# Optimization experiments

Measured on AMD Instinct MI355X. Metric: run time of the kernel, lower is better.

## Reference

```python
import jax, jax.numpy as jnp
import numpy as np

NUM_NODES = 50000
NUM_EDGES = 800000
INPUT_DIM = 256
OUTPUT_DIM = 256
NUM_HEADS = 8
HEAD_DIM = OUTPUT_DIM // NUM_HEADS


def setup_inputs() -> dict:
    key = jax.random.key(0)
    ks = jax.random.split(key, 14)
    x = jax.random.normal(ks[0], (NUM_NODES, INPUT_DIM), dtype=jnp.float32)
    edge_index = jax.random.randint(ks[1], (2, NUM_EDGES), 0, NUM_NODES, dtype=jnp.int32)
    # timestamps in seconds over ~11.5 days so log1p(|dt|/3600) is informative
    edge_time = jax.random.uniform(ks[2], (NUM_EDGES,), dtype=jnp.float32) * 1e6
    node_time = jax.random.uniform(ks[3], (NUM_NODES,), dtype=jnp.float32) * 1e6
    s_in = 1.0 / np.sqrt(INPUT_DIM)
    s_out = 1.0 / np.sqrt(OUTPUT_DIM)
    s_t = 1.0 / np.sqrt(2.0)
    Wq = jax.random.uniform(ks[4], (INPUT_DIM, OUTPUT_DIM), jnp.float32, -s_in, s_in)
    bq = jax.random.uniform(ks[5], (OUTPUT_DIM,), jnp.float32, -s_in, s_in)
    Wk = jax.random.uniform(ks[6], (INPUT_DIM, OUTPUT_DIM), jnp.float32, -s_in, s_in)
    bk = jax.random.uniform(ks[7], (OUTPUT_DIM,), jnp.float32, -s_in, s_in)
    Wv = jax.random.uniform(ks[8], (INPUT_DIM, OUTPUT_DIM), jnp.float32, -s_in, s_in)
    bv = jax.random.uniform(ks[9], (OUTPUT_DIM,), jnp.float32, -s_in, s_in)
    Wt = jax.random.uniform(ks[10], (2, NUM_HEADS), jnp.float32, -s_t, s_t)
    bt = jax.random.uniform(ks[11], (NUM_HEADS,), jnp.float32, -s_t, s_t)
    Wo = jax.random.uniform(ks[12], (OUTPUT_DIM, OUTPUT_DIM), jnp.float32, -s_out, s_out)
    bo = jax.random.uniform(ks[13], (OUTPUT_DIM,), jnp.float32, -s_out, s_out)
    return {"x": x, "edge_index": edge_index, "edge_time": edge_time, "node_time": node_time,
            "Wq": Wq, "bq": bq, "Wk": Wk, "bk": bk, "Wv": Wv, "bv": bv,
            "Wt": Wt, "bt": bt, "Wo": Wo, "bo": bo}


def reference(x, edge_index, edge_time, node_time, Wq, bq, Wk, bk, Wv, bv, Wt, bt, Wo, bo):
    n = x.shape[0]
    q = (x @ Wq + bq).reshape(n, NUM_HEADS, HEAD_DIM)
    k = (x @ Wk + bk).reshape(n, NUM_HEADS, HEAD_DIM)
    v = (x @ Wv + bv).reshape(n, NUM_HEADS, HEAD_DIM)
    src, dst = edge_index[0], edge_index[1]
    # temporal features per edge
    time_diff = edge_time - node_time[dst]
    time_features = jnp.stack(
        [jnp.sign(time_diff), jnp.log1p(jnp.abs(time_diff) / 3600.0)], axis=-1)  # [E, 2]
    temporal_weights = time_features @ Wt + bt  # [E, H]
    scale = HEAD_DIM ** -0.5
    scores = jnp.einsum('ehd,ehd->eh', q[dst], k[src]) * scale + temporal_weights  # [E, H]
    # softmax over ALL edges per head (dim=0), as in the original
    alpha = jax.nn.softmax(scores, axis=0)  # [E, H]
    msg = alpha[..., None] * v[src]  # [E, H, D]
    out = jax.ops.segment_sum(msg, dst, num_segments=n)  # [N, H, D]
    out = out.reshape(n, OUTPUT_DIM)
    return out @ Wo + bo
```

## Files before the change

### kernel.cpp

```cpp
#include <hip/hip_runtime.h>
#include <hip/hip_bf16.h>

#define NUM_NODES 50000
#define NUM_EDGES 800000
#define NUM_HEADS 8
#define HEAD_DIM 32
#define SCAN_BLOCKS 49
#define NCHUNK32 1563

typedef unsigned short ushort8 __attribute__((ext_vector_type(8)));
typedef float f32x4 __attribute__((ext_vector_type(4)));
typedef __bf16 bf16x8 __attribute__((ext_vector_type(8)));
typedef _Float16 h2 __attribute__((ext_vector_type(2)));

union BF8 { ushort8 u; bf16x8 b; };
union H8 { ushort8 u; h2 h[4]; };

#if defined(__has_builtin)
#if __has_builtin(__builtin_amdgcn_fdot2)
#define FDOT2(a, b, c) __builtin_amdgcn_fdot2((a), (b), (c), false)
#endif
#endif
#ifndef FDOT2
#define FDOT2(a, b, c) ((float)(a)[0] * (float)(b)[0] + (float)(a)[1] * (float)(b)[1] + (c))
#endif

__device__ __forceinline__ unsigned float_to_key(float f) {
    int i = __float_as_int(f);
    return (i >= 0) ? ((unsigned)i | 0x80000000u) : ~(unsigned)i;
}
__device__ __forceinline__ float key_to_float(unsigned u) {
    unsigned b = (u & 0x80000000u) ? (u & 0x7fffffffu) : ~u;
    return __int_as_float((int)b);
}
__device__ __forceinline__ float bf2f(unsigned short u) {
    return __uint_as_float(((unsigned)u) << 16);
}
__device__ __forceinline__ unsigned short f2bf(float f) {
    unsigned u = __float_as_uint(f);
    unsigned r = (u + 0x7fffu + ((u >> 16) & 1u)) >> 16;
    return (unsigned short)r;
}
__device__ __forceinline__ unsigned short f2h(float f) {
    _Float16 h = (_Float16)f;
    return *(unsigned short*)&h;
}

__global__ __launch_bounds__(256) void deg_kernel(const int* __restrict__ dst_idx, int* __restrict__ deg) {
    int e = blockIdx.x * 256 + threadIdx.x;
    if (e < NUM_EDGES) atomicAdd(&deg[dst_idx[e]], 1);
}

__global__ __launch_bounds__(1024) void scanA_kernel(
    const int* __restrict__ deg, int* __restrict__ offs, int* __restrict__ blocksum)
{
    __shared__ int buf[1024];
    int tid = threadIdx.x;
    int i = blockIdx.x * 1024 + tid;
    int v = (i < NUM_NODES) ? deg[i] : 0;
    buf[tid] = v;
    __syncthreads();
    for (int off = 1; off < 1024; off <<= 1) {
        int t = (tid >= off) ? buf[tid - off] : 0;
        __syncthreads();
        buf[tid] += t;
        __syncthreads();
    }
    if (i < NUM_NODES) offs[i] = buf[tid] - v;
    if (tid == 1023) blocksum[blockIdx.x] = buf[1023];
}

__global__ __launch_bounds__(64) void scanB_kernel(
    const int* __restrict__ blocksum, int* __restrict__ carry, int* __restrict__ offs)
{
    if (threadIdx.x == 0) {
        int acc = 0;
        for (int b = 0; b < SCAN_BLOCKS; b++) { carry[b] = acc; acc += blocksum[b]; }
        offs[NUM_NODES] = acc;
    }
}

__global__ __launch_bounds__(256) void scanC_kernel(
    int* __restrict__ offs, const int* __restrict__ carry, int* __restrict__ cursor)
{
    int i = blockIdx.x * 256 + threadIdx.x;
    if (i < NUM_NODES) {
        int v = offs[i] + carry[i >> 10];
        offs[i] = v;
        cursor[i] = v;
    }
}

__global__ __launch_bounds__(256) void fill3_kernel(
    const int* __restrict__ src_idx, const int* __restrict__ dst_idx,
    const float* __restrict__ edge_time, const float* __restrict__ node_time,
    int* __restrict__ cursor, int2* __restrict__ sd, float2* __restrict__ tf,
    int* __restrict__ src_s)
{
    int e = blockIdx.x * 256 + threadIdx.x;
    if (e < NUM_EDGES) {
        int d = dst_idx[e];
        int s = src_idx[e];
        int pos = atomicAdd(&cursor[d], 1);
        int2 v; v.x = s; v.y = d;
        sd[pos] = v;
        src_s[pos] = s;
        float td = edge_time[e] - node_time[d];
        float t0 = (td > 0.f) ? 1.f : ((td < 0.f) ? -1.f : 0.f);
        float t1 = log1pf(fabsf(td) * (1.f / 3600.f));
        tf[pos] = make_float2(t0, t1);
    }
}

__global__ __launch_bounds__(256) void wtrans_kernel(
    const float* __restrict__ Wq, const float* __restrict__ Wk,
    const float* __restrict__ Wv, const float* __restrict__ Wo,
    unsigned short* __restrict__ Wt)
{
    __shared__ float t[64][65];
    int nb = blockIdx.x * 64;
    int kb = blockIdx.y * 64;
    int g = nb >> 8;
    const float* W = (g == 0) ? Wq : (g == 1) ? Wk : (g == 2) ? Wv : Wo;
    int n0 = nb & 255;
    int tx = threadIdx.x & 63;
    int ty = threadIdx.x >> 6;
#pragma unroll
    for (int i = 0; i < 16; i++) {
        int k = i * 4 + ty;
        t[tx][k] = W[(size_t)(kb + k) * 256 + n0 + tx];
    }
    __syncthreads();
#pragma unroll
    for (int i = 0; i < 16; i++) {
        int n = i * 4 + ty;
        Wt[(size_t)(nb + n) * 256 + kb + tx] = f2bf(t[n][tx]);
    }
}

__global__ __launch_bounds__(256) void wpack_kernel(
    const unsigned short* __restrict__ Wt, unsigned short* __restrict__ Wpk)
{
    int gid = blockIdx.x * 256 + threadIdx.x;
    int lane = gid & 63;
    int fragidx = gid >> 6;
    int c2 = fragidx & 7;
    int nf = (fragidx >> 3) & 3;
    int cb = (fragidx >> 5) & 3;
    int g = fragidx >> 7;
    int l16 = lane & 15;
    int kg = lane >> 4;
    int n_col = g * 256 + cb * 64 + nf * 16 + l16;
    int k0 = c2 * 32 + kg * 8;
    ushort8 v = *(const ushort8*)(Wt + (size_t)n_col * 256 + k0);
    *(ushort8*)(Wpk + (size_t)gid * 8) = v;
}

__global__ __launch_bounds__(256) void gemm_qkv_mfma7(
    const float* __restrict__ A, int M,
    const unsigned short* __restrict__ Wpk,
    const float* __restrict__ b0, const float* __restrict__ b1, const float* __restrict__ b2,
    unsigned short* __restrict__ O0, unsigned short* __restrict__ O1, unsigned short* __restrict__ O2)
{
    __shared__ unsigned short As[64 * 256];
    int tid = threadIdx.x;
    int rowbase = blockIdx.x * 64;

    {
        int rsub = tid >> 6;
        int c4 = (tid & 63) * 4;
        int cchunk = (tid & 63) >> 1;
        int sub = (tid & 1);
#pragma unroll
        for (int it = 0; it < 16; it++) {
            int row = it * 4 + rsub;
            int grow = rowbase + row;
            float4 av = make_float4(0.f, 0.f, 0.f, 0.f);
            if (grow < M) av = *(const float4*)(A + (size_t)grow * 256 + c4);
            ushort4 o;
            o.x = f2bf(av.x); o.y = f2bf(av.y); o.z = f2bf(av.z); o.w = f2bf(av.w);
            unsigned byte = row * 512 + ((unsigned)(cchunk ^ (row & 7)) << 4) + sub * 8;
            *(ushort4*)((char*)As + byte) = o;
        }
    }
    __syncthreads();

    int lane = tid & 63;
    int wid = tid >> 6;
    int l16 = lane & 15;
    int kg = lane >> 4;

#pragma unroll
    for (int p = 0; p < 3; p++) {
        const float* bias = (p == 0) ? b0 : (p == 1) ? b1 : b2;
        unsigned short* O = (p == 0) ? O0 : (p == 1) ? O1 : O2;

        f32x4 acc[4][4];
#pragma unroll
        for (int m = 0; m < 4; m++)
#pragma unroll
            for (int n = 0; n < 4; n++) acc[m][n] = (f32x4)(0.0f);

        const ushort8* wbase = (const ushort8*)(Wpk + ((size_t)(p * 4 + wid) * 2048 + lane) * 8);

#pragma unroll
        for (int c2 = 0; c2 < 8; c2++) {
            bf16x8 wfr[4];
#pragma unroll
            for (int n = 0; n < 4; n++) {
                BF8 t; t.u = wbase[(n * 8 + c2) * 64];
                wfr[n] = t.b;
            }
            bf16x8 afr[4];
#pragma unroll
            for (int m = 0; m < 4; m++) {
                int row = m * 16 + l16;
                int cchunk = (c2 * 4 + kg) ^ (row & 7);
                BF8 t;
                t.u = *(const ushort8*)((const char*)As + row * 512 + (cchunk << 4));
                afr[m] = t.b;
            }
#pragma unroll
            for (int m = 0; m < 4; m++)
#pragma unroll
                for (int n = 0; n < 4; n++)
                    acc[m][n] = __builtin_amdgcn_mfma_f32_16x16x32_bf16(wfr[n], afr[m], acc[m][n], 0, 0, 0);
        }

#pragma unroll
        for (int m = 0; m < 4; m++) {
            int node = rowbase + m * 16 + l16;
            if (node >= M) continue;
#pragma unroll
            for (int n = 0; n < 4; n++) {
                int lc = wid * 64 + n * 16 + kg * 4;
                float4 bv = *(const float4*)(bias + lc);
                ushort4 o;
                if (p < 2) {
                    o.x = f2h(acc[m][n][0] + bv.x);
                    o.y = f2h(acc[m][n][1] + bv.y);
                    o.z = f2h(acc[m][n][2] + bv.z);
                    o.w = f2h(acc[m][n][3] + bv.w);
                } else {
                    o.x = f2bf(acc[m][n][0] + bv.x);
                    o.y = f2bf(acc[m][n][1] + bv.y);
                    o.z = f2bf(acc[m][n][2] + bv.z);
                    o.w = f2bf(acc[m][n][3] + bv.w);
                }
                int hh = lc >> 5, dd = lc & 31;
                *(ushort4*)(O + ((size_t)hh * NUM_NODES + node) * 32 + dd) = o;
            }
        }
    }
}

__global__ __launch_bounds__(256) void gemm_out_mfma6(
    const unsigned short* __restrict__ aggb, int M,
    const unsigned short* __restrict__ Wpk,
    const float* __restrict__ bias, const float* __restrict__ kscale,
    float* __restrict__ C)
{
    __shared__ unsigned short As[64 * 256];
    int tid = threadIdx.x;
    int rowbase = blockIdx.x * 64;

    {
        int rsub = tid >> 6;
        int c4 = (tid & 63) * 4;
        int cchunk = (tid & 63) >> 1;
        int sub = (tid & 1);
        int hh = c4 >> 5, dd = c4 & 31;
        float ks = kscale[hh];
#pragma unroll
        for (int it = 0; it < 16; it++) {
            int row = it * 4 + rsub;
            int grow = rowbase + row;
            ushort4 av = make_ushort4(0, 0, 0, 0);
            if (grow < M) av = *(const ushort4*)(aggb + ((size_t)hh * NUM_NODES + grow) * 32 + dd);
            ushort4 o;
            o.x = f2bf(bf2f(av.x) * ks); o.y = f2bf(bf2f(av.y) * ks);
            o.z = f2bf(bf2f(av.z) * ks); o.w = f2bf(bf2f(av.w) * ks);
            unsigned byte = row * 512 + ((unsigned)(cchunk ^ (row & 7)) << 4) + sub * 8;
            *(ushort4*)((char*)As + byte) = o;
        }
    }
    __syncthreads();

    int lane = tid & 63;
    int wid = tid >> 6;
    int l16 = lane & 15;
    int kg = lane >> 4;

    f32x4 acc[4][4];
#pragma unroll
    for (int m = 0; m < 4; m++)
#pragma unroll
        for (int n = 0; n < 4; n++) acc[m][n] = (f32x4)(0.0f);

    const ushort8* wbase = (const ushort8*)(Wpk + ((size_t)wid * 2048 + lane) * 8);

#pragma unroll
    for (int c2 = 0; c2 < 8; c2++) {
        bf16x8 wfr[4];
#pragma unroll
        for (int n = 0; n < 4; n++) {
            BF8 t; t.u = wbase[(n * 8 + c2) * 64];
            wfr[n] = t.b;
        }
        bf16x8 afr[4];
#pragma unroll
        for (int m = 0; m < 4; m++) {
            int row = m * 16 + l16;
            int cchunk = (c2 * 4 + kg) ^ (row & 7);
            BF8 t;
            t.u = *(const ushort8*)((const char*)As + row * 512 + (cchunk << 4));
            afr[m] = t.b;
        }
#pragma unroll
        for (int m = 0; m < 4; m++)
#pragma unroll
            for (int n = 0; n < 4; n++)
                acc[m][n] = __builtin_amdgcn_mfma_f32_16x16x32_bf16(wfr[n], afr[m], acc[m][n], 0, 0, 0);
    }

#pragma unroll
    for (int m = 0; m < 4; m++) {
        int node = rowbase + m * 16 + l16;
        if (node >= M) continue;
#pragma unroll
        for (int n = 0; n < 4; n++) {
            int col = wid * 64 + n * 16 + kg * 4;
            float4 bv = *(const float4*)(bias + col);
            float4 o;
            o.x = acc[m][n][0] + bv.x;
            o.y = acc[m][n][1] + bv.y;
            o.z = acc[m][n][2] + bv.z;
            o.w = acc[m][n][3] + bv.w;
            *(float4*)(C + (size_t)node * 256 + col) = o;
        }
    }
}

__global__ __launch_bounds__(256) void score4_kernel(
    const unsigned short* __restrict__ qh, const unsigned short* __restrict__ kh,
    const int2* __restrict__ sd, const float2* __restrict__ tf,
    const float* __restrict__ Wt, const float* __restrict__ bt,
    float* __restrict__ scores, unsigned* __restrict__ partialmax)
{
    __shared__ unsigned sm;
    int tid = threadIdx.x;
    if (tid == 0) sm = 0u;
    __syncthreads();
    int h = blockIdx.x & 7;
    int blk = blockIdx.x >> 3;
    float wt0 = Wt[h], wt1 = Wt[8 + h], btv = bt[h];
    const unsigned short* qhh = qh + (size_t)h * NUM_NODES * 32;
    const unsigned short* khh = kh + (size_t)h * NUM_NODES * 32;
    float* sc_h = scores + (size_t)h * NUM_EDGES;
    unsigned mykey = 0u;
    const int stride = 256 * 256;
    for (int pos = blk * 256 + tid; pos < NUM_EDGES; pos += stride) {
        int2 e = sd[pos];
        float2 t = tf[pos];
        const ushort8* qp = (const ushort8*)(qhh + (size_t)e.y * 32);
        const ushort8* kp = (const ushort8*)(khh + (size_t)e.x * 32);
        float dotv = 0.f;
#pragma unroll
        for (int i = 0; i < 4; i++) {
            H8 a, b;
            a.u = qp[i]; b.u = kp[i];
#pragma unroll
            for (int j = 0; j < 4; j++) dotv = FDOT2(a.h[j], b.h[j], dotv);
        }
        float sc = dotv * 0.17677669529663687f + (t.x * wt0 + t.y * wt1 + btv);
        sc_h[pos] = sc;
        unsigned kkey = float_to_key(sc);
        mykey = (kkey > mykey) ? kkey : mykey;
    }
#pragma unroll
    for (int off = 32; off > 0; off >>= 1) {
        unsigned o = __shfl_xor(mykey, off, 64);
        mykey = (o > mykey) ? o : mykey;
    }
    if ((tid & 63) == 0) atomicMax(&sm, mykey);
    __syncthreads();
    if (tid == 0) partialmax[blockIdx.x] = sm;
}

__global__ __launch_bounds__(256) void reduce_max3_kernel(
    const unsigned* __restrict__ partialmax, float* __restrict__ headmax)
{
    int tid = threadIdx.x;
    int h = tid >> 5, lane = tid & 31;
    unsigned m = 0u;
    for (int i = lane; i < 256; i += 32) {
        unsigned v = partialmax[i * 8 + h];
        m = (v > m) ? v : m;
    }
    for (int off = 16; off > 0; off >>= 1) {
        unsigned o = __shfl_down(m, off, 32);
        m = (o > m) ? o : m;
    }
    if (lane == 0) headmax[h] = key_to_float(m);
}

__global__ __launch_bounds__(256) void aggregate7_kernel(
    const unsigned short* __restrict__ vh, const float* __restrict__ scores,
    const int* __restrict__ src_s, const int* __restrict__ offs,
    const float* __restrict__ headmax, unsigned short* __restrict__ aggb,
    float* __restrict__ psum_part)
{
    __shared__ int sSrc[512];
    __shared__ float sP[512];
    __shared__ float blocksum;
    int tid = threadIdx.x;
    int h = blockIdx.x & 7;
    int chunk = blockIdx.x >> 3;
    int nodebase = chunk * 32;
    int g = tid >> 3;
    int ln = tid & 7;
    int node = nodebase + g;
    float m = headmax[h];
    const float* sc_h = scores + (size_t)h * NUM_EDGES;
    const unsigned short* vhh = vh + (size_t)h * NUM_NODES * 32;
    if (tid == 0) blocksum = 0.f;

    int blkstart = offs[nodebase];
    int blkend = offs[(nodebase + 32 < NUM_NODES) ? (nodebase + 32) : NUM_NODES];
    int start = 0, end = 0;
    if (node < NUM_NODES) { start = offs[node]; end = offs[node + 1]; }

    f32x4 a0 = (f32x4)(0.f), a1 = (f32x4)(0.f);
    float ps = 0.f;

    for (int t0 = blkstart; t0 < blkend; t0 += 512) {
        int cnt = min(512, blkend - t0);
        __syncthreads();
        for (int i = tid; i < cnt; i += 256) {
            sSrc[i] = src_s[t0 + i];
            float p = __expf(sc_h[t0 + i] - m);
            sP[i] = p;
            ps += p;
        }
        __syncthreads();
        int lo = (start > t0) ? start : t0;
        int hi = (end < t0 + cnt) ? end : (t0 + cnt);
        int cb = lo;
        for (; cb + 2 <= hi; cb += 2) {
            int i0 = cb - t0;
            int s0 = sSrc[i0], s1 = sSrc[i0 + 1];
            float p0 = sP[i0], p1 = sP[i0 + 1];
            ushort4 v0 = *(const ushort4*)(vhh + (size_t)s0 * 32 + ln * 4);
            ushort4 v1 = *(const ushort4*)(vhh + (size_t)s1 * 32 + ln * 4);
            a0[0] += p0 * bf2f(v0.x); a0[1] += p0 * bf2f(v0.y);
            a0[2] += p0 * bf2f(v0.z); a0[3] += p0 * bf2f(v0.w);
            a1[0] += p1 * bf2f(v1.x); a1[1] += p1 * bf2f(v1.y);
            a1[2] += p1 * bf2f(v1.z); a1[3] += p1 * bf2f(v1.w);
        }
        if (cb < hi) {
            int i0 = cb - t0;
            int s0 = sSrc[i0];
            float p0 = sP[i0];
            ushort4 v0 = *(const ushort4*)(vhh + (size_t)s0 * 32 + ln * 4);
            a0[0] += p0 * bf2f(v0.x); a0[1] += p0 * bf2f(v0.y);
            a0[2] += p0 * bf2f(v0.z); a0[3] += p0 * bf2f(v0.w);
        }
    }

    if (node < NUM_NODES) {
        ushort4 o;
        o.x = f2bf(a0[0] + a1[0]); o.y = f2bf(a0[1] + a1[1]);
        o.z = f2bf(a0[2] + a1[2]); o.w = f2bf(a0[3] + a1[3]);
        *(ushort4*)(aggb + ((size_t)h * NUM_NODES + node) * 32 + ln * 4) = o;
    }

    __syncthreads();
#pragma unroll
    for (int off = 32; off > 0; off >>= 1) ps += __shfl_xor(ps, off, 64);
    if ((tid & 63) == 0) atomicAdd(&blocksum, ps);
    __syncthreads();
    if (tid == 0) psum_part[blockIdx.x] = blocksum;
}

__global__ __launch_bounds__(256) void reduce_psum2_kernel(
    const float* __restrict__ psum_part, float* __restrict__ headinv)
{
    int tid = threadIdx.x;
    int h = tid >> 5, lane = tid & 31;
    float s = 0.f;
    for (int i = lane; i < NCHUNK32; i += 32) s += psum_part[i * 8 + h];
    for (int off = 16; off > 0; off >>= 1) s += __shfl_down(s, off, 32);
    if (lane == 0) headinv[h] = 1.f / s;
}

extern "C" void kernel_launch(void* const* d_in, const int* in_sizes, int n_in,
                              void* d_out, int out_size, void* d_ws, size_t ws_size,
                              hipStream_t stream) {
    const float* x = (const float*)d_in[0];
    const int* ei = (const int*)d_in[1];
    const int* src_idx = ei;
    const int* dst_idx = ei + NUM_EDGES;
    const float* edge_time = (const float*)d_in[2];
    const float* node_time = (const float*)d_in[3];
    const float* Wq = (const float*)d_in[4];  const float* bq = (const float*)d_in[5];
    const float* Wk = (const float*)d_in[6];  const float* bk = (const float*)d_in[7];
    const float* Wv = (const float*)d_in[8];  const float* bv = (const float*)d_in[9];
    const float* Wt = (const float*)d_in[10]; const float* bt = (const float*)d_in[11];
    const float* Wo = (const float*)d_in[12]; const float* bo = (const float*)d_in[13];
    float* out = (float*)d_out;

    char* w = (char*)d_ws;
    unsigned short* qb = (unsigned short*)w; w += (size_t)NUM_NODES * 256 * 2;
    unsigned short* kb = (unsigned short*)w; w += (size_t)NUM_NODES * 256 * 2;
    unsigned short* vb = (unsigned short*)w; w += (size_t)NUM_NODES * 256 * 2;
    float* scores = (float*)w;      w += (size_t)NUM_EDGES * 8 * 4;
    unsigned short* aggb = (unsigned short*)w; w += (size_t)NUM_NODES * 256 * 2;
    int2* sd = (int2*)w;            w += (size_t)NUM_EDGES * 8;
    float2* tfb = (float2*)w;       w += (size_t)NUM_EDGES * 8;
    int* src_s = (int*)w;           w += (size_t)NUM_EDGES * 4;
    int* deg = (int*)w;             w += (size_t)NUM_NODES * 4;
    int* offs = (int*)w;            w += (size_t)(NUM_NODES + 1) * 4;
    int* cursor = (int*)w;          w += (size_t)NUM_NODES * 4;
    unsigned* partialmax = (unsigned*)w; w += 2048 * 4;
    float* psum_part = (float*)w;   w += (size_t)NCHUNK32 * 8 * 4;
    float* headmax = (float*)w;     w += 8 * 4;
    float* headinv = (float*)w;     w += 8 * 4;
    int* blocksum = (int*)w;        w += 64 * 4;
    int* bcarry = (int*)w;          w += 64 * 4;
    unsigned short* Wtb = (unsigned short*)w; w += (size_t)1024 * 256 * 2;
    unsigned short* Wpk = (unsigned short*)w; w += (size_t)1024 * 256 * 2;

    hipMemsetAsync(deg, 0, (size_t)NUM_NODES * 4, stream);

    dim3 gw(16, 4);
    wtrans_kernel<<<gw, 256, 0, stream>>>(Wq, Wk, Wv, Wo, Wtb);
    wpack_kernel<<<128, 256, 0, stream>>>(Wtb, Wpk);

    deg_kernel<<<(NUM_EDGES + 255) / 256, 256, 0, stream>>>(dst_idx, deg);
    scanA_kernel<<<SCAN_BLOCKS, 1024, 0, stream>>>(deg, offs, blocksum);
    scanB_kernel<<<1, 64, 0, stream>>>(blocksum, bcarry, offs);
    scanC_kernel<<<(NUM_NODES + 255) / 256, 256, 0, stream>>>(offs, bcarry, cursor);
    fill3_kernel<<<(NUM_EDGES + 255) / 256, 256, 0, stream>>>(
        src_idx, dst_idx, edge_time, node_time, cursor, sd, tfb, src_s);

    gemm_qkv_mfma7<<<(NUM_NODES + 63) / 64, 256, 0, stream>>>(
        x, NUM_NODES, Wpk, bq, bk, bv, qb, kb, vb);

    score4_kernel<<<2048, 256, 0, stream>>>(qb, kb, sd, tfb, Wt, bt, scores, partialmax);
    reduce_max3_kernel<<<1, 256, 0, stream>>>(partialmax, headmax);

    aggregate7_kernel<<<NCHUNK32 * 8, 256, 0, stream>>>(
        vb, scores, src_s, offs, headmax, aggb, psum_part);
    reduce_psum2_kernel<<<1, 256, 0, stream>>>(psum_part, headinv);

    gemm_out_mfma6<<<(NUM_NODES + 63) / 64, 256, 0, stream>>>(
        aggb, NUM_NODES, Wpk + (size_t)768 * 256, bo, headinv, out);
}
```

Baseline: 347.2 us.

## Split CSR fill into index scatter and coalesced gather, pack time features as fp16

The single scatter-fill kernel becomes two. The first only records each edge's sorted position. The second walks sorted positions and gathers source, destination and time data, so its writes are coalesced instead of scattered. Time features are packed as two fp16 values in one 32-bit word instead of a float2, and the separate src_s array is dropped in favour of reading sd.x in aggregation. This adds an extra launch and a gather pass, lowers the precision of the temporal features, and aggregation now reads 8-byte sd entries to use 4 bytes.

```diff
diff --git a/kernel.cpp b/kernel.cpp
--- a/kernel.cpp
+++ b/kernel.cpp
@@ -45,6 +45,10 @@
     _Float16 h = (_Float16)f;
     return *(unsigned short*)&h;
 }
+__device__ __forceinline__ float h2f(unsigned short u) {
+    _Float16 h = *(const _Float16*)&u;
+    return (float)h;
+}
 
 __global__ __launch_bounds__(256) void deg_kernel(const int* __restrict__ dst_idx, int* __restrict__ deg) {
     int e = blockIdx.x * 256 + threadIdx.x;
@@ -91,24 +95,33 @@
     }
 }
 
-__global__ __launch_bounds__(256) void fill3_kernel(
+__global__ __launch_bounds__(256) void fillA_kernel(
+    const int* __restrict__ dst_idx, int* __restrict__ cursor, int* __restrict__ edge_of)
+{
+    int e = blockIdx.x * 256 + threadIdx.x;
+    if (e < NUM_EDGES) {
+        int pos = atomicAdd(&cursor[dst_idx[e]], 1);
+        edge_of[pos] = e;
+    }
+}
+
+__global__ __launch_bounds__(256) void fillB_kernel(
+    const int* __restrict__ edge_of,
     const int* __restrict__ src_idx, const int* __restrict__ dst_idx,
     const float* __restrict__ edge_time, const float* __restrict__ node_time,
-    int* __restrict__ cursor, int2* __restrict__ sd, float2* __restrict__ tf,
-    int* __restrict__ src_s)
-{
-    int e = blockIdx.x * 256 + threadIdx.x;
-    if (e < NUM_EDGES) {
+    int2* __restrict__ sd, unsigned* __restrict__ tfh)
+{
+    int pos = blockIdx.x * 256 + threadIdx.x;
+    if (pos < NUM_EDGES) {
+        int e = edge_of[pos];
+        int s = src_idx[e];
         int d = dst_idx[e];
-        int s = src_idx[e];
-        int pos = atomicAdd(&cursor[d], 1);
         int2 v; v.x = s; v.y = d;
         sd[pos] = v;
-        src_s[pos] = s;
         float td = edge_time[e] - node_time[d];
         float t0 = (td > 0.f) ? 1.f : ((td < 0.f) ? -1.f : 0.f);
         float t1 = log1pf(fabsf(td) * (1.f / 3600.f));
-        tf[pos] = make_float2(t0, t1);
+        tfh[pos] = (unsigned)f2h(t0) | ((unsigned)f2h(t1) << 16);
     }
 }
 
@@ -341,9 +354,9 @@
     }
 }
 
-__global__ __launch_bounds__(256) void score4_kernel(
+__global__ __launch_bounds__(256) void score5_kernel(
     const unsigned short* __restrict__ qh, const unsigned short* __restrict__ kh,
-    const int2* __restrict__ sd, const float2* __restrict__ tf,
+    const int2* __restrict__ sd, const unsigned* __restrict__ tfh,
     const float* __restrict__ Wt, const float* __restrict__ bt,
     float* __restrict__ scores, unsigned* __restrict__ partialmax)
 {
@@ -361,7 +374,9 @@
     const int stride = 256 * 256;
     for (int pos = blk * 256 + tid; pos < NUM_EDGES; pos += stride) {
         int2 e = sd[pos];
-        float2 t = tf[pos];
+        unsigned tp = tfh[pos];
+        float t0 = h2f((unsigned short)(tp & 0xffffu));
+        float t1 = h2f((unsigned short)(tp >> 16));
         const ushort8* qp = (const ushort8*)(qhh + (size_t)e.y * 32);
         const ushort8* kp = (const ushort8*)(khh + (size_t)e.x * 32);
         float dotv = 0.f;
@@ -372,7 +387,7 @@
 #pragma unroll
             for (int j = 0; j < 4; j++) dotv = FDOT2(a.h[j], b.h[j], dotv);
         }
-        float sc = dotv * 0.17677669529663687f + (t.x * wt0 + t.y * wt1 + btv);
+        float sc = dotv * 0.17677669529663687f + (t0 * wt0 + t1 * wt1 + btv);
         sc_h[pos] = sc;
         unsigned kkey = float_to_key(sc);
         mykey = (kkey > mykey) ? kkey : mykey;
@@ -404,9 +419,9 @@
     if (lane == 0) headmax[h] = key_to_float(m);
 }
 
-__global__ __launch_bounds__(256) void aggregate7_kernel(
+__global__ __launch_bounds__(256) void aggregate8_kernel(
     const unsigned short* __restrict__ vh, const float* __restrict__ scores,
-    const int* __restrict__ src_s, const int* __restrict__ offs,
+    const int2* __restrict__ sd, const int* __restrict__ offs,
     const float* __restrict__ headmax, unsigned short* __restrict__ aggb,
     float* __restrict__ psum_part)
 {
@@ -437,7 +452,7 @@
         int cnt = min(512, blkend - t0);
         __syncthreads();
         for (int i = tid; i < cnt; i += 256) {
-            sSrc[i] = src_s[t0 + i];
+            sSrc[i] = sd[t0 + i].x;
             float p = __expf(sc_h[t0 + i] - m);
             sP[i] = p;
             ps += p;
@@ -516,8 +531,8 @@
     float* scores = (float*)w;      w += (size_t)NUM_EDGES * 8 * 4;
     unsigned short* aggb = (unsigned short*)w; w += (size_t)NUM_NODES * 256 * 2;
     int2* sd = (int2*)w;            w += (size_t)NUM_EDGES * 8;
-    float2* tfb = (float2*)w;       w += (size_t)NUM_EDGES * 8;
-    int* src_s = (int*)w;           w += (size_t)NUM_EDGES * 4;
+    unsigned* tfh = (unsigned*)w;   w += (size_t)NUM_EDGES * 4;
+    int* edge_of = (int*)w;         w += (size_t)NUM_EDGES * 4;
     int* deg = (int*)w;             w += (size_t)NUM_NODES * 4;
     int* offs = (int*)w;            w += (size_t)(NUM_NODES + 1) * 4;
     int* cursor = (int*)w;          w += (size_t)NUM_NODES * 4;
@@ -540,17 +555,18 @@
     scanA_kernel<<<SCAN_BLOCKS, 1024, 0, stream>>>(deg, offs, blocksum);
     scanB_kernel<<<1, 64, 0, stream>>>(blocksum, bcarry, offs);
     scanC_kernel<<<(NUM_NODES + 255) / 256, 256, 0, stream>>>(offs, bcarry, cursor);
-    fill3_kernel<<<(NUM_EDGES + 255) / 256, 256, 0, stream>>>(
-        src_idx, dst_idx, edge_time, node_time, cursor, sd, tfb, src_s);
+    fillA_kernel<<<(NUM_EDGES + 255) / 256, 256, 0, stream>>>(dst_idx, cursor, edge_of);
+    fillB_kernel<<<(NUM_EDGES + 255) / 256, 256, 0, stream>>>(
+        edge_of, src_idx, dst_idx, edge_time, node_time, sd, tfh);
 
     gemm_qkv_mfma7<<<(NUM_NODES + 63) / 64, 256, 0, stream>>>(
         x, NUM_NODES, Wpk, bq, bk, bv, qb, kb, vb);
 
-    score4_kernel<<<2048, 256, 0, stream>>>(qb, kb, sd, tfb, Wt, bt, scores, partialmax);
+    score5_kernel<<<2048, 256, 0, stream>>>(qb, kb, sd, tfh, Wt, bt, scores, partialmax);
     reduce_max3_kernel<<<1, 256, 0, stream>>>(partialmax, headmax);
 
-    aggregate7_kernel<<<NCHUNK32 * 8, 256, 0, stream>>>(
-        vb, scores, src_s, offs, headmax, aggb, psum_part);
+    aggregate8_kernel<<<NCHUNK32 * 8, 256, 0, stream>>>(
+        vb, scores, sd, offs, headmax, aggb, psum_part);
     reduce_psum2_kernel<<<1, 256, 0, stream>>>(psum_part, headinv);
 
     gemm_out_mfma6<<<(NUM_NODES + 63) / 64, 256, 0, stream>>>(
```

Result: slower. 369.3 us (+6.4%).
